# Optimization experiments

Measured on AMD Instinct MI355X. Metric: run time of the kernel, lower is better.

The kernel has to match this reference:

```python
import jax, jax.numpy as jnp
import numpy as np

N = 100000   # nodes
E = 1600000  # edges per view
F = 256      # feature_dim
G = 512      # num graphs in batch
H, C = 2, 32 # heads, channels per head (GATConv(F, 32, heads=2))
EPS = 1e-5


def setup_inputs() -> dict:
    key = jax.random.key(0)
    ks = jax.random.split(key, 32)
    def w(i, shape, fan_in):
        return jax.random.normal(ks[i], shape, jnp.float32) / np.sqrt(fan_in)
    inp = {
        "x": jax.random.normal(ks[0], (N, F), jnp.float32),
        "edge_index_ast": jax.random.randint(ks[1], (2, E), 0, N),
        "edge_index_cfg": jax.random.randint(ks[2], (2, E), 0, N),
        "edge_index_pdg": jax.random.randint(ks[3], (2, E), 0, N),
        "batch": jnp.sort(jax.random.randint(ks[4], (N,), 0, G)),
        "num_graphs": G,
        # BatchNorm1d(feature_dim) affine params (training-mode batch stats)
        "bn_w": jnp.ones((F,), jnp.float32),
        "bn_b": jnp.zeros((F,), jnp.float32),
    }
    i = 5
    for v in ("ast", "cfg", "pdg"):
        inp[f"{v}_W"] = w(i, (F, H * C), F); i += 1
        inp[f"{v}_att_src"] = w(i, (H, C), C); i += 1
        inp[f"{v}_att_dst"] = w(i, (H, C), C); i += 1
        inp[f"{v}_bias"] = jnp.zeros((H * C,), jnp.float32)
    inp["g1_w"] = w(i, (64, 32), 64); i += 1
    inp["g1_b"] = jnp.zeros((32,), jnp.float32)
    inp["g2_w"] = w(i, (32, 3), 32); i += 1
    inp["g2_b"] = jnp.zeros((3,), jnp.float32)
    inp["c1_w"] = w(i, (64, 128), 64); i += 1
    inp["c1_b"] = jnp.zeros((128,), jnp.float32)
    inp["c2_w"] = w(i, (128, 64), 128); i += 1
    inp["c2_b"] = jnp.zeros((64,), jnp.float32)
    inp["c3_w"] = w(i, (64, 1), 64); i += 1
    inp["c3_b"] = jnp.zeros((1,), jnp.float32)
    return inp


def _gat(x, edge_index, W, att_src, att_dst, bias):
    """PyG GATConv (shared lin, add_self_loops=True, concat heads)."""
    n = x.shape[0]
    loops = jnp.arange(n)
    src = jnp.concatenate([edge_index[0], loops])
    dst = jnp.concatenate([edge_index[1], loops])
    h = (x @ W).reshape(n, H, C)                       # [N,H,C]
    a_src = jnp.sum(h * att_src, axis=-1)              # [N,H]
    a_dst = jnp.sum(h * att_dst, axis=-1)              # [N,H]
    e = jax.nn.leaky_relu(a_src[src] + a_dst[dst], 0.2)  # [Etot,H]
    m = jax.ops.segment_max(e, dst, num_segments=n)
    p = jnp.exp(e - m[dst])
    denom = jax.ops.segment_sum(p, dst, num_segments=n)
    alpha = p / (denom[dst] + 1e-16)                   # [Etot,H]
    out = jax.ops.segment_sum(h[src] * alpha[:, :, None], dst, num_segments=n)
    return out.reshape(n, H * C) + bias


def reference(x, edge_index_ast, edge_index_cfg, edge_index_pdg, batch, num_graphs,
              bn_w, bn_b,
              ast_W, ast_att_src, ast_att_dst, ast_bias,
              cfg_W, cfg_att_src, cfg_att_dst, cfg_bias,
              pdg_W, pdg_att_src, pdg_att_dst, pdg_bias,
              g1_w, g1_b, g2_w, g2_b,
              c1_w, c1_b, c2_w, c2_b, c3_w, c3_b):
    # input BatchNorm1d (training-mode batch statistics, biased variance)
    mu = x.mean(0)
    var = x.var(0)
    xn = (x - mu) / jnp.sqrt(var + EPS) * bn_w + bn_b

    h_ast = jax.ops.segment_max(jax.nn.elu(_gat(xn, edge_index_ast, ast_W, ast_att_src, ast_att_dst, ast_bias)), batch, num_segments=num_graphs)
    h_cfg = jax.ops.segment_max(jax.nn.elu(_gat(xn, edge_index_cfg, cfg_W, cfg_att_src, cfg_att_dst, cfg_bias)), batch, num_segments=num_graphs)
    h_pdg = jax.ops.segment_max(jax.nn.elu(_gat(xn, edge_index_pdg, pdg_W, pdg_att_src, pdg_att_dst, pdg_bias)), batch, num_segments=num_graphs)

    avg_view = (h_ast + h_cfg + h_pdg) / 3.0
    wts = jax.nn.softmax(jax.nn.relu(avg_view @ g1_w + g1_b) @ g2_w + g2_b, axis=-1)
    fused = wts[:, 0:1] * h_ast + wts[:, 1:2] * h_cfg + wts[:, 2:3] * h_pdg

    # classifier (dropout = identity at inference)
    z = jax.nn.relu(fused @ c1_w + c1_b)
    z = jax.nn.relu(z @ c2_w + c2_b)
    logits = (z @ c3_w + c3_b).reshape(-1)             # [G]
    return logits
```

## Files before the change

### kernel.cpp

```cpp
#include <hip/hip_runtime.h>
#include <hip/hip_bf16.h>
#include <hip/hip_fp16.h>

#define N_NODES 100000
#define N_EDGES 1600000
#define ETOT    (N_EDGES + N_NODES)
#define NE3     (3 * ETOT)
#define N3      (3 * N_NODES)
#define NF      256
#define NG      512
#define NHC     64
#define NOUT3   192
#define BN_EPS  1e-5f

#define NBUCK   293
#define NB1     1024
#define EGRAIN  20
#define ECHUNK  (256 * EGRAIN)
#define SCAN_N  (NBUCK * NB1)
#define ATT_NB  (N3 * 16 / 256)

typedef _Float16 f16x8 __attribute__((ext_vector_type(8)));
typedef float    f32x4 __attribute__((ext_vector_type(4)));

__device__ __forceinline__ unsigned fenc(float f){
  unsigned b = __float_as_uint(f);
  return (b & 0x80000000u) ? ~b : (b | 0x80000000u);
}
__device__ __forceinline__ float fdec(unsigned u){
  unsigned b = (u & 0x80000000u) ? (u & 0x7FFFFFFFu) : ~u;
  return __uint_as_float(b);
}
__device__ __forceinline__ float lrelu(float x){ return x > 0.f ? x : 0.2f * x; }
__device__ __forceinline__ float eluf(float x){ return x > 0.f ? x : (__expf(x) - 1.f); }

__global__ void k_init_pooled(unsigned* pooled){
  int i = blockIdx.x * 256 + threadIdx.x;
  if (i < 3 * NG * NHC) pooled[i] = 0x007FFFFFu;
}

#define STATS_NB ((N_NODES + 127) / 128)
__global__ __launch_bounds__(256) void k_pre(const float* __restrict__ x,
                                             float* __restrict__ spartS, float* __restrict__ spartQ,
                                             const int* __restrict__ eA, const int* __restrict__ eC,
                                             const int* __restrict__ eP,
                                             int* __restrict__ gcounts){
  int t = threadIdx.x;
  if (blockIdx.x < STATS_NB){
    int r0 = blockIdx.x * 128;
    int rmax = N_NODES - r0; if (rmax > 128) rmax = 128;
    float s = 0.f, q = 0.f;
    for (int r = 0; r < rmax; ++r){
      float v = x[(size_t)(r0 + r) * NF + t];
      s += v; q += v * v;
    }
    spartS[(size_t)t * STATS_NB + blockIdx.x] = s;
    spartQ[(size_t)t * STATS_NB + blockIdx.x] = q;
    return;
  }
  __shared__ int hist[NBUCK];
  int bi = blockIdx.x - STATS_NB;
  for (int b = t; b < NBUCK; b += 256) hist[b] = 0;
  __syncthreads();
  int base = bi * ECHUNK + t;
#pragma unroll
  for (int k = 0; k < EGRAIN; ++k){
    int i = base + k * 256;
    if (i < NE3){
      int v = i / ETOT; int j = i - v * ETOT;
      const int* ei = (v == 0) ? eA : (v == 1) ? eC : eP;
      int d = (j < N_EDGES) ? ei[N_EDGES + j] : (j - N_EDGES);
      int vd = v * N_NODES + d;
      atomicAdd(&hist[vd >> 10], 1);
    }
  }
  __syncthreads();
  for (int b = t; b < NBUCK; b += 256) gcounts[b * NB1 + bi] = hist[b];
}

__global__ __launch_bounds__(256) void k_stats2(const float* __restrict__ spartS, const float* __restrict__ spartQ,
                                                float* __restrict__ sums, float* __restrict__ sumsq){
  __shared__ float rs[256], rq[256];
  int c = blockIdx.x, i = threadIdx.x;
  float s = 0.f, q = 0.f;
  for (int b = i; b < STATS_NB; b += 256){
    s += spartS[(size_t)c * STATS_NB + b];
    q += spartQ[(size_t)c * STATS_NB + b];
  }
  rs[i] = s; rq[i] = q;
  __syncthreads();
  for (int off = 128; off > 0; off >>= 1){
    if (i < off){ rs[i] += rs[i + off]; rq[i] += rq[i + off]; }
    __syncthreads();
  }
  if (i == 0){ sums[c] = rs[0]; sumsq[c] = rq[0]; }
}

__global__ __launch_bounds__(256) void k_prep2(const float* __restrict__ sums, const float* __restrict__ sumsq,
                                               const float* __restrict__ bn_w, const float* __restrict__ bn_b,
                                               const float* __restrict__ WA, const float* __restrict__ WC,
                                               const float* __restrict__ WP,
                                               __half* __restrict__ WpT, float* __restrict__ bp){
  __shared__ float red[256];
  int o = blockIdx.x;
  int v = o >> 6, oc = o & 63;
  const float* W = (v == 0) ? WA : (v == 1) ? WC : WP;
  int f = threadIdx.x;
  float mu  = sums[f]  * (1.f / N_NODES);
  float var = sumsq[f] * (1.f / N_NODES) - mu * mu;
  float sc  = bn_w[f] * rsqrtf(var + BN_EPS);
  float sh_ = bn_b[f] - mu * sc;
  float w = W[f * 64 + oc];
  WpT[(size_t)o * NF + f] = __float2half(w * sc);
  red[f] = sh_ * w;
  __syncthreads();
  for (int off = 128; off > 0; off >>= 1){
    if (f < off) red[f] += red[f + off];
    __syncthreads();
  }
  if (f == 0) bp[o] = red[0];
}

__global__ __launch_bounds__(256) void k_scan1(const int* __restrict__ cnt, int* __restrict__ out,
                                               int* __restrict__ bsum, int n){
  __shared__ int sh[256];
  int t = threadIdx.x; int base = blockIdx.x * 2048 + t * 8;
  int v[8]; int s = 0;
#pragma unroll
  for (int i = 0; i < 8; ++i){ v[i] = (base + i < n) ? cnt[base + i] : 0; s += v[i]; }
  sh[t] = s; __syncthreads();
  for (int off = 1; off < 256; off <<= 1){
    int xv = (t >= off) ? sh[t - off] : 0;
    __syncthreads();
    sh[t] += xv;
    __syncthreads();
  }
  int p = sh[t] - s;
  if (t == 255) bsum[blockIdx.x] = sh[255];
#pragma unroll
  for (int i = 0; i < 8; ++i){ if (base + i < n) out[base + i] = p; p += v[i]; }
}

__global__ __launch_bounds__(512) void k_scan2(int* __restrict__ bsum, int* __restrict__ total_out, int nb){
  __shared__ int sh[512];
  int t = threadIdx.x;
  int o = (t < nb) ? bsum[t] : 0;
  sh[t] = o; __syncthreads();
  for (int off = 1; off < 512; off <<= 1){
    int xv = (t >= off) ? sh[t - off] : 0;
    __syncthreads();
    sh[t] += xv;
    __syncthreads();
  }
  if (t < nb) bsum[t] = sh[t] - o;
  if (t == nb - 1) total_out[0] = sh[t];
}

__global__ __launch_bounds__(256) void k_scan3(int* __restrict__ out, const int* __restrict__ bsum, int n){
  int add = bsum[blockIdx.x];
  int base = blockIdx.x * 2048 + threadIdx.x * 8;
#pragma unroll
  for (int i = 0; i < 8; ++i) if (base + i < n) out[base + i] += add;
}

#define GBM 64
#define GEMM_NB ((N_NODES + GBM - 1) / GBM)
__global__ __launch_bounds__(256) void k_fused(const float* __restrict__ x,
                                               const __half* __restrict__ WpT, const float* __restrict__ bp,
                                               __half* __restrict__ h16,
                                               const int* __restrict__ eA, const int* __restrict__ eC,
                                               const int* __restrict__ eP,
                                               const int* __restrict__ gscan, int* __restrict__ packed){
  union U { _Float16 xs[64 * 256]; int pos[NBUCK]; };
  __shared__ U sm;
  int t = threadIdx.x;
  if (blockIdx.x >= GEMM_NB){
    int bi = blockIdx.x - GEMM_NB;
    for (int b = t; b < NBUCK; b += 256) sm.pos[b] = gscan[b * NB1 + bi];
    __syncthreads();
    int base = bi * ECHUNK + t;
#pragma unroll
    for (int k = 0; k < EGRAIN; ++k){
      int i = base + k * 256;
      if (i < NE3){
        int v = i / ETOT; int j = i - v * ETOT;
        const int* ei = (v == 0) ? eA : (v == 1) ? eC : eP;
        int s, d;
        if (j < N_EDGES){ s = ei[j]; d = ei[N_EDGES + j]; } else { s = j - N_EDGES; d = s; }
        int vd = v * N_NODES + d;
        int p = atomicAdd(&sm.pos[vd >> 10], 1);
        packed[p] = s | ((vd & 1023) << 17);
      }
    }
    return;
  }
  int m0 = blockIdx.x * GBM;
#pragma unroll
  for (int k = 0; k < 8; ++k){
    int G = t + k * 256;
    int row = G >> 5, g = G & 31;
    int grow = m0 + row; if (grow >= N_NODES) grow = N_NODES - 1;
    const float4* src = (const float4*)(x + (size_t)grow * NF + ((g ^ (row & 7)) << 3));
    float4 lo = src[0], hi = src[1];
    f16x8 h;
    h[0]=(_Float16)lo.x; h[1]=(_Float16)lo.y; h[2]=(_Float16)lo.z; h[3]=(_Float16)lo.w;
    h[4]=(_Float16)hi.x; h[5]=(_Float16)hi.y; h[6]=(_Float16)hi.z; h[7]=(_Float16)hi.w;
    *(f16x8*)&sm.xs[(size_t)G << 3] = h;
  }
  __syncthreads();
  int lane = t & 63, w = t >> 6;
  int lr = lane & 15, lk = lane >> 4;
  int colb = w * 48;
  f32x4 acc[4][3];
#pragma unroll
  for (int mt = 0; mt < 4; ++mt)
#pragma unroll
    for (int ct = 0; ct < 3; ++ct) acc[mt][ct] = (f32x4){0.f, 0.f, 0.f, 0.f};
  float bpv[3];
#pragma unroll
  for (int ct = 0; ct < 3; ++ct) bpv[ct] = bp[colb + ct * 16 + lr];
#pragma unroll
  for (int kk = 0; kk < 8; ++kk){
    int khalf = kk * 32 + lk * 8;
    f16x8 av[4];
#pragma unroll
    for (int mt = 0; mt < 4; ++mt){
      int row = mt * 16 + lr;
      av[mt] = *(const f16x8*)&sm.xs[row * 256 + (khalf ^ ((row & 7) << 3))];
    }
    f16x8 bv[3];
#pragma unroll
    for (int ct = 0; ct < 3; ++ct){
      int col = colb + ct * 16 + lr;
      bv[ct] = *(const f16x8*)(const void*)(WpT + (size_t)col * NF + khalf);
    }
#pragma unroll
    for (int mt = 0; mt < 4; ++mt)
#pragma unroll
      for (int ct = 0; ct < 3; ++ct)
        acc[mt][ct] = __builtin_amdgcn_mfma_f32_16x16x32_f16(av[mt], bv[ct], acc[mt][ct], 0, 0, 0);
  }
#pragma unroll
  for (int mt = 0; mt < 4; ++mt){
#pragma unroll
    for (int r = 0; r < 4; ++r){
      int row = m0 + mt * 16 + lk * 4 + r;
      if (row < N_NODES){
#pragma unroll
        for (int ct = 0; ct < 3; ++ct)
          h16[(size_t)row * NOUT3 + colb + ct * 16 + lr] = __float2half(acc[mt][ct][r] + bpv[ct]);
      }
    }
  }
}

__global__ __launch_bounds__(256) void k_att(const __half* __restrict__ h16,
                                             const float* __restrict__ asA, const float* __restrict__ adA,
                                             const float* __restrict__ asC, const float* __restrict__ adC,
                                             const float* __restrict__ asP, const float* __restrict__ adP,
                                             float* __restrict__ a_src, float* __restrict__ a_dst,
                                             unsigned* __restrict__ gpart){
  __shared__ unsigned samax[6];
  int t = threadIdx.x;
  if (t < 6) samax[t] = 0u;
  __syncthreads();
  int gt = blockIdx.x * 256 + t;
  int g = gt >> 4; int lid = gt & 15;
  int v = g / N_NODES; int n = g - v * N_NODES;
  const float* As = (v == 0) ? asA : (v == 1) ? asC : asP;
  const float* Ad = (v == 0) ? adA : (v == 1) ? adC : adP;
  const __half2* hp = (const __half2*)(h16 + (size_t)n * NOUT3 + v * 64 + lid * 4);
  float2 fa = __half22float2(hp[0]);
  float2 fb = __half22float2(hp[1]);
  float4 s4 = *(const float4*)(As + lid * 4);
  float4 d4 = *(const float4*)(Ad + lid * 4);
  float rs = fa.x*s4.x + fa.y*s4.y + fb.x*s4.z + fb.y*s4.w;
  float rd = fa.x*d4.x + fa.y*d4.y + fb.x*d4.z + fb.y*d4.w;
  rs += __shfl_xor(rs, 1); rd += __shfl_xor(rd, 1);
  rs += __shfl_xor(rs, 2); rd += __shfl_xor(rd, 2);
  rs += __shfl_xor(rs, 4); rd += __shfl_xor(rd, 4);
  if ((lid & 7) == 0){
    int h = lid >> 3;
    a_src[g * 2 + h] = rs;
    a_dst[g * 2 + h] = rd;
    atomicMax(&samax[v * 2 + h], fenc(rs));
  }
  __syncthreads();
  if (t < 6) gpart[blockIdx.x * 6 + t] = samax[t];
}

__global__ __launch_bounds__(512) void k_build(const int* __restrict__ gscan, const int* __restrict__ packed,
                                               int* __restrict__ entries, int* __restrict__ offsets,
                                               const unsigned* __restrict__ gpart, unsigned* __restrict__ amax){
  __shared__ int hist2[1024];
  __shared__ int sh[512];
  __shared__ unsigned smx[6];
  int b = blockIdx.x, t = threadIdx.x;
  if (b == 0){
    if (t < 6) smx[t] = 0u;
    __syncthreads();
    unsigned m[6] = {0u, 0u, 0u, 0u, 0u, 0u};
    for (int bi = t; bi < ATT_NB; bi += 512){
      const unsigned* p = gpart + (size_t)bi * 6;
#pragma unroll
      for (int k = 0; k < 6; ++k) m[k] = max(m[k], p[k]);
    }
#pragma unroll
    for (int k = 0; k < 6; ++k) atomicMax(&smx[k], m[k]);
    __syncthreads();
    if (t < 6) amax[t] = smx[t];
  }
  int base = gscan[b * NB1];
  int end  = (b == NBUCK - 1) ? NE3 : gscan[(b + 1) * NB1];
  hist2[t * 2] = 0; hist2[t * 2 + 1] = 0;
  __syncthreads();
  for (int i = base + t; i < end; i += 512)
    atomicAdd(&hist2[(packed[i] >> 17) & 1023], 1);
  __syncthreads();
  int s0 = hist2[t * 2], s1 = hist2[t * 2 + 1];
  int tot = s0 + s1;
  sh[t] = tot; __syncthreads();
  for (int off = 1; off < 512; off <<= 1){
    int xv = (t >= off) ? sh[t - off] : 0;
    __syncthreads();
    sh[t] += xv;
    __syncthreads();
  }
  int excl = sh[t] - tot;
  hist2[t * 2]     = excl;
  hist2[t * 2 + 1] = excl + s0;
  int vd0 = (b << 10) + t * 2;
  if (vd0 < N3)     offsets[vd0]     = base + excl;
  if (vd0 + 1 < N3) offsets[vd0 + 1] = base + excl + s0;
  if (b == NBUCK - 1 && t == 0) offsets[N3] = NE3;
  __syncthreads();
  for (int i = base + t; i < end; i += 512){
    int pk = packed[i];
    int low = (pk >> 17) & 1023;
    int pos = atomicAdd(&hist2[low], 1);
    entries[base + pos] = pk & 0x1FFFF;
  }
}

__global__ __launch_bounds__(256) void k_gather(const int* __restrict__ entries, const int* __restrict__ offsets,
                                                const float* __restrict__ a_src, const float* __restrict__ a_dst,
                                                const unsigned* __restrict__ amax,
                                                const __half* __restrict__ h16,
                                                const float* __restrict__ bA, const float* __restrict__ bC,
                                                const float* __restrict__ bP,
                                                const int* __restrict__ batch, unsigned* __restrict__ pooled){
  __shared__ unsigned red[64];
  __shared__ int kmin, kmax;
  int t = threadIdx.x;
  if (t == 0){ kmin = 0x7FFFFFFF; kmax = -1; }
  if (t < 64) red[t] = 0u;
  __syncthreads();
  int grp = t >> 4;
  int lid = t & 15;
  int g = blockIdx.x * 16 + grp;
  int v = g / N_NODES; int n = g - v * N_NODES;
  int vN = v * N_NODES;
  float ad0 = a_dst[g*2+0], ad1 = a_dst[g*2+1];
  float m0 = lrelu(fdec(amax[v*2+0]) + ad0);
  float m1 = lrelu(fdec(amax[v*2+1]) + ad1);
  int beg = offsets[g], end = offsets[g+1];
  int len = end - beg;
  float ax = 0.f, ay = 0.f, az = 0.f, aw = 0.f;
  float den0 = 0.f, den1 = 0.f;
  const char* hb = (const char*)h16;
  unsigned lconst = (unsigned)((v << 7) + (lid << 3));
  for (int c0 = 0; c0 < len; c0 += 16){
    int nc = len - c0; if (nc > 16) nc = 16;
    unsigned off_ = 0u;
    float p0f = 0.f, p1f = 0.f;
    if (lid < nc){
      int s_ = entries[beg + c0 + lid];
      float2 ap = *(const float2*)(a_src + (size_t)(vN + s_) * 2);
      p0f = __expf(lrelu(ap.x + ad0) - m0);
      p1f = __expf(lrelu(ap.y + ad1) - m1);
      off_ = (unsigned)s_ * (NOUT3 * 2);
    }
    den0 += p0f; den1 += p1f;
    for (int k = 0; k < nc; k += 8){
      uint2 r[8]; float pa[8];
#pragma unroll
      for (int j = 0; j < 8; ++j){
        int kk = k + j;
        unsigned ob = (unsigned)__shfl((int)off_, kk, 16) + lconst;
        float pA = __shfl(p0f, kk, 16);
        float pB = __shfl(p1f, kk, 16);
        r[j] = *(const uint2*)(hb + ob);
        pa[j] = (lid < 8) ? pA : pB;
      }
#pragma unroll
      for (int j = 0; j < 8; ++j){
        float2 fa2 = __half22float2(*(__half2*)&r[j].x);
        float2 fb2 = __half22float2(*(__half2*)&r[j].y);
        ax = fmaf(pa[j], fa2.x, ax); ay = fmaf(pa[j], fa2.y, ay);
        az = fmaf(pa[j], fb2.x, az); aw = fmaf(pa[j], fb2.y, aw);
      }
    }
  }
#pragma unroll
  for (int msk = 1; msk < 16; msk <<= 1){
    den0 += __shfl_xor(den0, msk);
    den1 += __shfl_xor(den1, msk);
  }
  float den = ((lid < 8) ? den0 : den1) + 1e-16f;
  const float* bias = (v == 0) ? bA : (v == 1) ? bC : bP;
  float4 b4 = *(const float4*)(bias + lid * 4);
  unsigned e0u = fenc(eluf(ax / den + b4.x));
  unsigned e1u = fenc(eluf(ay / den + b4.y));
  unsigned e2u = fenc(eluf(az / den + b4.z));
  unsigned e3u = fenc(eluf(aw / den + b4.w));
  int key = v * NG + batch[n];
  if (lid == 0){ atomicMin(&kmin, key); atomicMax(&kmax, key); }
  atomicMax(&red[lid*4+0], e0u); atomicMax(&red[lid*4+1], e1u);
  atomicMax(&red[lid*4+2], e2u); atomicMax(&red[lid*4+3], e3u);
  __syncthreads();
  if (kmin == kmax){
    if (t < 64) atomicMax(&pooled[(size_t)kmin * 64 + t], red[t]);
  } else {
    unsigned* pp = pooled + (size_t)key * 64 + lid * 4;
    atomicMax(pp+0, e0u); atomicMax(pp+1, e1u); atomicMax(pp+2, e2u); atomicMax(pp+3, e3u);
  }
}

__global__ __launch_bounds__(64) void k_head(const unsigned* __restrict__ pooled,
                                             const float* __restrict__ g1w, const float* __restrict__ g1b,
                                             const float* __restrict__ g2w, const float* __restrict__ g2b,
                                             const float* __restrict__ c1w, const float* __restrict__ c1b,
                                             const float* __restrict__ c2w, const float* __restrict__ c2b,
                                             const float* __restrict__ c3w, const float* __restrict__ c3b,
                                             float* __restrict__ out){
  __shared__ float s1[64];
  __shared__ float s2[128];
  __shared__ float sw[3];
  int g = blockIdx.x, l = threadIdx.x;
  float ha = fdec(pooled[(size_t)g * 64 + l]);
  float hc = fdec(pooled[(size_t)(NG + g) * 64 + l]);
  float hp = fdec(pooled[(size_t)(2 * NG + g) * 64 + l]);
  s1[l] = (ha + hc + hp) * (1.f / 3.f);
  __syncthreads();
  float r1 = 0.f;
  if (l < 32){
    r1 = g1b[l];
    for (int i = 0; i < 64; ++i) r1 += s1[i] * g1w[i * 32 + l];
    r1 = fmaxf(r1, 0.f);
  }
  __syncthreads();
  if (l < 32) s2[l] = r1;
  __syncthreads();
  if (l < 3){
    float tv = g2b[l];
    for (int i = 0; i < 32; ++i) tv += s2[i] * g2w[i * 3 + l];
    sw[l] = tv;
  }
  __syncthreads();
  float t0 = sw[0], t1 = sw[1], t2 = sw[2];
  float mx = fmaxf(t0, fmaxf(t1, t2));
  float w0 = __expf(t0 - mx), w1 = __expf(t1 - mx), w2 = __expf(t2 - mx);
  float wsum = w0 + w1 + w2;
  float fused = (w0 * ha + w1 * hc + w2 * hp) / wsum;
  __syncthreads();
  s1[l] = fused;
  __syncthreads();
  float za = c1b[l], zb = c1b[64 + l];
  for (int i = 0; i < 64; ++i){
    float f = s1[i];
    za += f * c1w[i * 128 + l];
    zb += f * c1w[i * 128 + 64 + l];
  }
  za = fmaxf(za, 0.f); zb = fmaxf(zb, 0.f);
  s2[l] = za; s2[64 + l] = zb;
  __syncthreads();
  float z2 = c2b[l];
  for (int i = 0; i < 128; ++i) z2 += s2[i] * c2w[i * 64 + l];
  z2 = fmaxf(z2, 0.f);
  float prod = z2 * c3w[l];
  for (int off = 32; off > 0; off >>= 1) prod += __shfl_down(prod, off);
  if (l == 0) out[g] = prod + c3b[0];
}

extern "C" void kernel_launch(void* const* d_in, const int* in_sizes, int n_in,
                              void* d_out, int out_size, void* d_ws, size_t ws_size,
                              hipStream_t stream){
  const float* x    = (const float*)d_in[0];
  const int* eA     = (const int*)d_in[1];
  const int* eC     = (const int*)d_in[2];
  const int* eP     = (const int*)d_in[3];
  const int* batch  = (const int*)d_in[4];
  const float* bn_w = (const float*)d_in[6];
  const float* bn_b = (const float*)d_in[7];
  const float* WA   = (const float*)d_in[8];
  const float* asA  = (const float*)d_in[9];
  const float* adA  = (const float*)d_in[10];
  const float* bA   = (const float*)d_in[11];
  const float* WC   = (const float*)d_in[12];
  const float* asC  = (const float*)d_in[13];
  const float* adC  = (const float*)d_in[14];
  const float* bC   = (const float*)d_in[15];
  const float* WP   = (const float*)d_in[16];
  const float* asP  = (const float*)d_in[17];
  const float* adP  = (const float*)d_in[18];
  const float* bP   = (const float*)d_in[19];
  const float* g1w  = (const float*)d_in[20];
  const float* g1b  = (const float*)d_in[21];
  const float* g2w  = (const float*)d_in[22];
  const float* g2b  = (const float*)d_in[23];
  const float* c1w  = (const float*)d_in[24];
  const float* c1b  = (const float*)d_in[25];
  const float* c2w  = (const float*)d_in[26];
  const float* c2b  = (const float*)d_in[27];
  const float* c3w  = (const float*)d_in[28];
  const float* c3b  = (const float*)d_in[29];
  float* out = (float*)d_out;

  char* wptr = (char*)d_ws;
  auto alloc = [&](size_t bytes) -> void* {
    void* p = (void*)wptr;
    wptr += (bytes + 255) & ~(size_t)255;
    return p;
  };
  float*    sums    = (float*)   alloc((size_t)NF * 4);
  float*    sumsq   = (float*)   alloc((size_t)NF * 4);
  float*    spartS  = (float*)   alloc((size_t)NF * STATS_NB * 4);
  float*    spartQ  = (float*)   alloc((size_t)NF * STATS_NB * 4);
  int*      gcounts = (int*)     alloc((size_t)SCAN_N * 4);
  int*      gscan   = (int*)     alloc((size_t)SCAN_N * 4);
  int*      offsets = (int*)     alloc(((size_t)N3 + 1) * 4);
  __half*   WpT     = (__half*)  alloc((size_t)NOUT3 * NF * 2);
  float*    bp      = (float*)   alloc((size_t)NOUT3 * 4);
  __half*   h16     = (__half*)  alloc((size_t)N_NODES * NOUT3 * 2);
  float*    a_src   = (float*)   alloc((size_t)N3 * 2 * 4);
  float*    a_dst   = (float*)   alloc((size_t)N3 * 2 * 4);
  int*      packed  = (int*)     alloc((size_t)NE3 * 4);
  int*      entries = (int*)     alloc((size_t)NE3 * 4);
  unsigned* pooled  = (unsigned*)alloc((size_t)3 * NG * NHC * 4);
  unsigned* gpart   = (unsigned*)alloc((size_t)ATT_NB * 6 * 4);
  unsigned* amax    = (unsigned*)alloc((size_t)64 * 4);
  int*      bsum    = (int*)     alloc((size_t)512 * 4);
  int*      scrtot  = (int*)     alloc((size_t)64 * 4);

  k_init_pooled<<<(3 * NG * NHC + 255) / 256, 256, 0, stream>>>(pooled);
  k_pre<<<STATS_NB + NB1, 256, 0, stream>>>(x, spartS, spartQ, eA, eC, eP, gcounts);
  k_stats2<<<NF, 256, 0, stream>>>(spartS, spartQ, sums, sumsq);
  k_prep2<<<NOUT3, 256, 0, stream>>>(sums, sumsq, bn_w, bn_b, WA, WC, WP, WpT, bp);
  int nb_sc = (SCAN_N + 2047) / 2048;
  k_scan1<<<nb_sc, 256, 0, stream>>>(gcounts, gscan, bsum, SCAN_N);
  k_scan2<<<1, 512, 0, stream>>>(bsum, scrtot, nb_sc);
  k_scan3<<<nb_sc, 256, 0, stream>>>(gscan, bsum, SCAN_N);
  k_fused<<<GEMM_NB + NB1, 256, 0, stream>>>(x, WpT, bp, h16, eA, eC, eP, gscan, packed);
  k_att<<<ATT_NB, 256, 0, stream>>>(h16, asA, adA, asC, adC, asP, adP, a_src, a_dst, gpart);
  k_build<<<NBUCK, 512, 0, stream>>>(gscan, packed, entries, offsets, gpart, amax);
  k_gather<<<N3 / 16, 256, 0, stream>>>(entries, offsets, a_src, a_dst, amax, h16, bA, bC, bP, batch, pooled);
  k_head<<<NG, 64, 0, stream>>>(pooled, g1w, g1b, g2w, g2b, c1w, c1b, c2w, c2b, c3w, c3b, out);
}
```

Measured before the change: 330.2 us.

## Fold pooled init into k_pre, interleave fused blocks, pack attention weights as half2

Drops the separate pooled-initialisation kernel by adding extra blocks to k_pre, which saves one launch. k_fused now interleaves GEMM blocks and edge-scatter blocks in a 3:2 pattern, so the compute-bound and memory-bound work share the GPU at the same time instead of the scatter running at the tail. In the gather kernel, the two per-edge softmax weights are packed as fp16 into one 32-bit value, needing one shuffle instead of two per edge. In exchange the weights lose precision, and the denominator is summed from the rounded values to stay consistent with the numerator.

```diff
diff --git a/kernel.cpp b/kernel.cpp
--- a/kernel.cpp
+++ b/kernel.cpp
@@ -19,6 +19,7 @@
 #define ECHUNK  (256 * EGRAIN)
 #define SCAN_N  (NBUCK * NB1)
 #define ATT_NB  (N3 * 16 / 256)
+#define INIT_NB ((3 * NG * NHC + 255) / 256)
 
 typedef _Float16 f16x8 __attribute__((ext_vector_type(8)));
 typedef float    f32x4 __attribute__((ext_vector_type(4)));
@@ -33,19 +34,19 @@
 }
 __device__ __forceinline__ float lrelu(float x){ return x > 0.f ? x : 0.2f * x; }
 __device__ __forceinline__ float eluf(float x){ return x > 0.f ? x : (__expf(x) - 1.f); }
-
-__global__ void k_init_pooled(unsigned* pooled){
-  int i = blockIdx.x * 256 + threadIdx.x;
-  if (i < 3 * NG * NHC) pooled[i] = 0x007FFFFFu;
-}
 
 #define STATS_NB ((N_NODES + 127) / 128)
 __global__ __launch_bounds__(256) void k_pre(const float* __restrict__ x,
                                              float* __restrict__ spartS, float* __restrict__ spartQ,
                                              const int* __restrict__ eA, const int* __restrict__ eC,
                                              const int* __restrict__ eP,
-                                             int* __restrict__ gcounts){
+                                             int* __restrict__ gcounts, unsigned* __restrict__ pooled){
   int t = threadIdx.x;
+  if (blockIdx.x >= STATS_NB + NB1){
+    int i = (blockIdx.x - STATS_NB - NB1) * 256 + t;
+    if (i < 3 * NG * NHC) pooled[i] = 0x007FFFFFu;
+    return;
+  }
   if (blockIdx.x < STATS_NB){
     int r0 = blockIdx.x * 128;
     int rmax = N_NODES - r0; if (rmax > 128) rmax = 128;
@@ -165,6 +166,8 @@
 
 #define GBM 64
 #define GEMM_NB ((N_NODES + GBM - 1) / GBM)
+#define NGRP5   521
+#define FUSED_NB (NGRP5 * 5)
 __global__ __launch_bounds__(256) void k_fused(const float* __restrict__ x,
                                                const __half* __restrict__ WpT, const float* __restrict__ bp,
                                                __half* __restrict__ h16,
@@ -174,8 +177,10 @@
   union U { _Float16 xs[64 * 256]; int pos[NBUCK]; };
   __shared__ U sm;
   int t = threadIdx.x;
-  if (blockIdx.x >= GEMM_NB){
-    int bi = blockIdx.x - GEMM_NB;
+  int grp5 = blockIdx.x / 5, rem5 = blockIdx.x % 5;
+  if (rem5 >= 3){
+    int bi = grp5 * 2 + (rem5 - 3);
+    if (bi >= NB1) return;
     for (int b = t; b < NBUCK; b += 256) sm.pos[b] = gscan[b * NB1 + bi];
     __syncthreads();
     int base = bi * ECHUNK + t;
@@ -194,7 +199,9 @@
     }
     return;
   }
-  int m0 = blockIdx.x * GBM;
+  int gb = grp5 * 3 + rem5;
+  if (gb >= GEMM_NB) return;
+  int m0 = gb * GBM;
 #pragma unroll
   for (int k = 0; k < 8; ++k){
     int G = t + k * 256;
@@ -371,26 +378,28 @@
   unsigned lconst = (unsigned)((v << 7) + (lid << 3));
   for (int c0 = 0; c0 < len; c0 += 16){
     int nc = len - c0; if (nc > 16) nc = 16;
-    unsigned off_ = 0u;
-    float p0f = 0.f, p1f = 0.f;
+    unsigned off_ = 0u, pu_ = 0u;
     if (lid < nc){
       int s_ = entries[beg + c0 + lid];
       float2 ap = *(const float2*)(a_src + (size_t)(vN + s_) * 2);
-      p0f = __expf(lrelu(ap.x + ad0) - m0);
-      p1f = __expf(lrelu(ap.y + ad1) - m1);
+      float p0 = __expf(lrelu(ap.x + ad0) - m0);
+      float p1 = __expf(lrelu(ap.y + ad1) - m1);
+      pu_ = (unsigned)__half_as_ushort(__float2half(p0))
+          | ((unsigned)__half_as_ushort(__float2half(p1)) << 16);
       off_ = (unsigned)s_ * (NOUT3 * 2);
     }
-    den0 += p0f; den1 += p1f;
+    den0 += __half2float(__ushort_as_half((unsigned short)(pu_ & 0xFFFFu)));
+    den1 += __half2float(__ushort_as_half((unsigned short)(pu_ >> 16)));
     for (int k = 0; k < nc; k += 8){
       uint2 r[8]; float pa[8];
 #pragma unroll
       for (int j = 0; j < 8; ++j){
         int kk = k + j;
         unsigned ob = (unsigned)__shfl((int)off_, kk, 16) + lconst;
-        float pA = __shfl(p0f, kk, 16);
-        float pB = __shfl(p1f, kk, 16);
+        unsigned pk_ = (unsigned)__shfl((int)pu_, kk, 16);
         r[j] = *(const uint2*)(hb + ob);
-        pa[j] = (lid < 8) ? pA : pB;
+        unsigned sel = (lid < 8) ? (pk_ & 0xFFFFu) : (pk_ >> 16);
+        pa[j] = __half2float(__ushort_as_half((unsigned short)sel));
       }
 #pragma unroll
       for (int j = 0; j < 8; ++j){
@@ -542,15 +551,14 @@
   int*      bsum    = (int*)     alloc((size_t)512 * 4);
   int*      scrtot  = (int*)     alloc((size_t)64 * 4);
 
-  k_init_pooled<<<(3 * NG * NHC + 255) / 256, 256, 0, stream>>>(pooled);
-  k_pre<<<STATS_NB + NB1, 256, 0, stream>>>(x, spartS, spartQ, eA, eC, eP, gcounts);
+  k_pre<<<STATS_NB + NB1 + INIT_NB, 256, 0, stream>>>(x, spartS, spartQ, eA, eC, eP, gcounts, pooled);
   k_stats2<<<NF, 256, 0, stream>>>(spartS, spartQ, sums, sumsq);
   k_prep2<<<NOUT3, 256, 0, stream>>>(sums, sumsq, bn_w, bn_b, WA, WC, WP, WpT, bp);
   int nb_sc = (SCAN_N + 2047) / 2048;
   k_scan1<<<nb_sc, 256, 0, stream>>>(gcounts, gscan, bsum, SCAN_N);
   k_scan2<<<1, 512, 0, stream>>>(bsum, scrtot, nb_sc);
   k_scan3<<<nb_sc, 256, 0, stream>>>(gscan, bsum, SCAN_N);
-  k_fused<<<GEMM_NB + NB1, 256, 0, stream>>>(x, WpT, bp, h16, eA, eC, eP, gscan, packed);
+  k_fused<<<FUSED_NB, 256, 0, stream>>>(x, WpT, bp, h16, eA, eC, eP, gscan, packed);
   k_att<<<ATT_NB, 256, 0, stream>>>(h16, asA, adA, asC, adC, asP, adP, a_src, a_dst, gpart);
   k_build<<<NBUCK, 512, 0, stream>>>(gscan, packed, entries, offsets, gpart, amax);
   k_gather<<<N3 / 16, 256, 0, stream>>>(entries, offsets, a_src, a_dst, amax, h16, bA, bC, bP, batch, pooled);
```

Measured after the change: 327.7 us. About the same (-0.8%).
